# Optimization experiments

Hardware: AMD Instinct MI355X
Metric: run time of the kernel (lower is better)

The kernel has to match this reference:

```python
import jax, jax.numpy as jnp
import numpy as np
import math

NX = 4096   # input features (last_dim)
NY = 4096   # units
REDUCTION = 0.5  # param_reduction


def _make_window(nx, ny, reduction):
    """Faithful vectorized port of SzDense.build for form='diagonal', halfbandwidth=0."""
    hw = nx * ny / math.sqrt(nx * nx + ny * ny) * (1.0 - math.sqrt(reduction))
    rxy = (nx - 1) / (ny - 1)
    hwdiv = hw * math.sqrt(rxy * rxy + 1.0)
    iy = np.arange(ny, dtype=np.float64)
    c1 = rxy * iy - hwdiv
    # int(c1)+1 when c1>=0 (truncation == floor for nonneg), else 0
    ix1 = np.where(c1 >= 0, np.floor(c1).astype(np.int64) + 1, 0)
    c2 = rxy * iy + hwdiv
    ix2 = np.where(c2 < nx, np.ceil(c2).astype(np.int64), nx)
    ix = np.arange(nx)[:, None]
    wnd = ((ix >= ix1[None, :]) & (ix < ix2[None, :])).astype(np.float32)
    num_ones = float(wnd.sum())
    w_corr = (nx * ny) / num_ones if num_ones > 0 else 1.0
    return wnd, np.float32(w_corr)


def setup_inputs() -> dict:
    key = jax.random.key(0)
    kx, kk, kb = jax.random.split(key, 3)
    x = jax.random.normal(kx, (4096, NX), dtype=jnp.float32)
    wnd_np, w_corr = _make_window(NX, NY, REDUCTION)
    window = jnp.asarray(wnd_np)
    # glorot-uniform-like init, then build()'s kernel.assign(kernel * wnd * w_corr)
    limit = math.sqrt(6.0 / (NX + NY))
    kernel = jax.random.uniform(kk, (NX, NY), dtype=jnp.float32, minval=-limit, maxval=limit)
    kernel = kernel * window * w_corr
    bias = jnp.zeros((NY,), dtype=jnp.float32)
    return {"x": x, "kernel": kernel, "window": window, "bias": bias}


def reference(x, kernel, window, bias):
    # SzDense.call: dense(inputs, kernel * window, bias, activation=None)
    return jnp.matmul(x, kernel * window) + bias
```

## Files before the change

kernel.cpp:

```cpp
#include <hip/hip_runtime.h>
#include <hip/hip_bf16.h>
#include <stdint.h>

#define MM 4096
#define NN 4096
#define KK 4096
#define BM 128
#define BN 128
#define BK 32

typedef __bf16 bf16;
typedef __attribute__((ext_vector_type(8))) __bf16 bf16x8;
typedef __attribute__((ext_vector_type(4))) __bf16 bf16x4;
typedef __attribute__((ext_vector_type(4))) float f32x4;

__device__ inline const __attribute__((address_space(1))) void* to_global(const void* p) {
    return (const __attribute__((address_space(1))) void*)p;
}
__device__ inline __attribute__((address_space(3))) void* to_local(void* p) {
    return (__attribute__((address_space(3))) void*)p;
}

__global__ void convert_x(const float* __restrict__ x, bf16* __restrict__ out) {
    size_t i = ((size_t)blockIdx.x * blockDim.x + threadIdx.x) * 8;
    float4 v0 = *(const float4*)(x + i);
    float4 v1 = *(const float4*)(x + i + 4);
    bf16x8 o;
    o[0] = (bf16)v0.x; o[1] = (bf16)v0.y; o[2] = (bf16)v0.z; o[3] = (bf16)v0.w;
    o[4] = (bf16)v1.x; o[5] = (bf16)v1.y; o[6] = (bf16)v1.z; o[7] = (bf16)v1.w;
    *(bf16x8*)(out + i) = o;
}

#define LDN 68
__global__ void convert_wt(const float* __restrict__ w, const float* __restrict__ wnd,
                           bf16* __restrict__ bt) {
    __shared__ bf16 Ts[64][LDN];
    const int t = threadIdx.x;
    const int k0 = blockIdx.y * 64;
    const int n0 = blockIdx.x * 64;

    {
        const int nc = (t & 15) * 4;
        const int kb = t >> 4;
        #pragma unroll
        for (int p = 0; p < 4; ++p) {
            const int kl = p * 16 + kb;
            size_t idx = (size_t)(k0 + kl) * NN + (n0 + nc);
            float4 a = *(const float4*)(w + idx);
            float4 b = *(const float4*)(wnd + idx);
            bf16x4 o;
            o[0] = (bf16)(a.x * b.x);
            o[1] = (bf16)(a.y * b.y);
            o[2] = (bf16)(a.z * b.z);
            o[3] = (bf16)(a.w * b.w);
            *(bf16x4*)&Ts[kl][nc] = o;
        }
    }
    __syncthreads();

    {
        const int nl = t >> 2;
        #pragma unroll
        for (int p = 0; p < 2; ++p) {
            const int kc = (t & 3) + 4 * p;
            bf16x8 o;
            #pragma unroll
            for (int i = 0; i < 8; ++i) o[i] = Ts[kc * 8 + i][nl];
            *(bf16x8*)&bt[(size_t)(n0 + nl) * KK + k0 + kc * 8] = o;
        }
    }
}

__global__ __launch_bounds__(256, 3) void gemm_bt_bias(
    const bf16* __restrict__ A,
    const bf16* __restrict__ Bt,
    const float* __restrict__ bias,
    float* __restrict__ C) {
    __shared__ bf16 As[BM * BK];
    __shared__ bf16 Bs[BN * BK];

    const int t = threadIdx.x;
    const int wave = t >> 6;
    const int lane = t & 63;
    const int quad = lane >> 4;
    const int l15 = lane & 15;
    const int m0 = blockIdx.y * BM;
    const int n0 = blockIdx.x * BN;
    const int wm = wave >> 1;
    const int wn = wave & 1;

    f32x4 acc[4][4];
    #pragma unroll
    for (int i = 0; i < 4; ++i)
        #pragma unroll
        for (int j = 0; j < 4; ++j)
            acc[i][j] = (f32x4)0.0f;

    const int row_a0 = t >> 2;
    const int col_a0 = (t & 3) * 8;
    const bf16* Ag = A + (size_t)(m0 + row_a0) * KK + col_a0;
    const bf16* Bg = Bt + (size_t)(n0 + row_a0) * KK + col_a0;

    for (int k0 = 0; k0 < KK; k0 += BK) {
        #pragma unroll
        for (int c = 0; c < 2; ++c) {
            __builtin_amdgcn_global_load_lds(
                to_global(Ag + k0 + (size_t)c * 64 * KK),
                to_local(As + ((size_t)c * 256 + wave * 64) * 8), 16, 0, 0);
            __builtin_amdgcn_global_load_lds(
                to_global(Bg + k0 + (size_t)c * 64 * KK),
                to_local(Bs + ((size_t)c * 256 + wave * 64) * 8), 16, 0, 0);
        }
        __syncthreads();

        bf16x8 af[4], bfr[4];
        #pragma unroll
        for (int i = 0; i < 4; ++i)
            af[i] = *(const bf16x8*)&As[(wm * 64 + i * 16 + l15) * BK + quad * 8];
        #pragma unroll
        for (int j = 0; j < 4; ++j)
            bfr[j] = *(const bf16x8*)&Bs[(wn * 64 + j * 16 + l15) * BK + quad * 8];

        #pragma unroll
        for (int i = 0; i < 4; ++i)
            #pragma unroll
            for (int j = 0; j < 4; ++j)
                acc[i][j] = __builtin_amdgcn_mfma_f32_16x16x32_bf16(af[i], bfr[j], acc[i][j], 0, 0, 0);

        __syncthreads();
    }

    #pragma unroll
    for (int i = 0; i < 4; ++i) {
        #pragma unroll
        for (int j = 0; j < 4; ++j) {
            int col = n0 + wn * 64 + j * 16 + l15;
            float b = bias[col];
            #pragma unroll
            for (int r = 0; r < 4; ++r) {
                int row = m0 + wm * 64 + i * 16 + quad * 4 + r;
                C[(size_t)row * NN + col] = acc[i][j][r] + b;
            }
        }
    }
}

extern "C" void kernel_launch(void* const* d_in, const int* in_sizes, int n_in,
                              void* d_out, int out_size, void* d_ws, size_t ws_size,
                              hipStream_t stream) {
    const float* x = (const float*)d_in[0];
    const float* kern = (const float*)d_in[1];
    const float* wnd = (const float*)d_in[2];
    const float* bias = (const float*)d_in[3];
    float* out = (float*)d_out;

    bf16* Abf = (bf16*)d_ws;
    bf16* Btbf = (bf16*)((char*)d_ws + (size_t)MM * KK * sizeof(bf16));

    convert_x<<<(MM * (size_t)KK / 8 + 255) / 256, 256, 0, stream>>>(x, Abf);
    convert_wt<<<dim3(NN / 64, KK / 64), 256, 0, stream>>>(kern, wnd, Btbf);
    gemm_bt_bias<<<dim3(NN / BN, MM / BM), 256, 0, stream>>>(Abf, Btbf, bias, out);
}
```

Baseline: 360.9 us.

## Merge conversion kernels and remap GEMM tiles for per-XCD L2 locality

Merges the x conversion and the masked weight transpose into one launch, with the block index choosing which job each block does, which removes one kernel launch and the gap between launches. Remaps GEMM block indices so each XCD (blocks assigned round-robin by flat index) works on a contiguous group of four N tiles, so B tiles are reused within that XCD's L2. Raises the launch-bounds occupancy hint from 3 to 4 waves per SIMD, which may add register pressure or spills.

```diff
diff --git a/kernel.cpp b/kernel.cpp
--- a/kernel.cpp
+++ b/kernel.cpp
@@ -21,23 +21,29 @@
     return (__attribute__((address_space(3))) void*)p;
 }
 
-__global__ void convert_x(const float* __restrict__ x, bf16* __restrict__ out) {
-    size_t i = ((size_t)blockIdx.x * blockDim.x + threadIdx.x) * 8;
-    float4 v0 = *(const float4*)(x + i);
-    float4 v1 = *(const float4*)(x + i + 4);
-    bf16x8 o;
-    o[0] = (bf16)v0.x; o[1] = (bf16)v0.y; o[2] = (bf16)v0.z; o[3] = (bf16)v0.w;
-    o[4] = (bf16)v1.x; o[5] = (bf16)v1.y; o[6] = (bf16)v1.z; o[7] = (bf16)v1.w;
-    *(bf16x8*)(out + i) = o;
-}
-
 #define LDN 68
-__global__ void convert_wt(const float* __restrict__ w, const float* __restrict__ wnd,
-                           bf16* __restrict__ bt) {
+#define NBX 8192
+__global__ void prep(const float* __restrict__ x,
+                     const float* __restrict__ w,
+                     const float* __restrict__ wnd,
+                     bf16* __restrict__ Abf,
+                     bf16* __restrict__ bt) {
     __shared__ bf16 Ts[64][LDN];
     const int t = threadIdx.x;
-    const int k0 = blockIdx.y * 64;
-    const int n0 = blockIdx.x * 64;
+    int b = blockIdx.x;
+    if (b < NBX) {
+        size_t i = ((size_t)b * 256 + t) * 8;
+        float4 v0 = *(const float4*)(x + i);
+        float4 v1 = *(const float4*)(x + i + 4);
+        bf16x8 o;
+        o[0] = (bf16)v0.x; o[1] = (bf16)v0.y; o[2] = (bf16)v0.z; o[3] = (bf16)v0.w;
+        o[4] = (bf16)v1.x; o[5] = (bf16)v1.y; o[6] = (bf16)v1.z; o[7] = (bf16)v1.w;
+        *(bf16x8*)(Abf + i) = o;
+        return;
+    }
+    b -= NBX;
+    const int k0 = (b >> 6) * 64;
+    const int n0 = (b & 63) * 64;
 
     {
         const int nc = (t & 15) * 4;
@@ -47,12 +53,12 @@
             const int kl = p * 16 + kb;
             size_t idx = (size_t)(k0 + kl) * NN + (n0 + nc);
             float4 a = *(const float4*)(w + idx);
-            float4 b = *(const float4*)(wnd + idx);
+            float4 m = *(const float4*)(wnd + idx);
             bf16x4 o;
-            o[0] = (bf16)(a.x * b.x);
-            o[1] = (bf16)(a.y * b.y);
-            o[2] = (bf16)(a.z * b.z);
-            o[3] = (bf16)(a.w * b.w);
+            o[0] = (bf16)(a.x * m.x);
+            o[1] = (bf16)(a.y * m.y);
+            o[2] = (bf16)(a.z * m.z);
+            o[3] = (bf16)(a.w * m.w);
             *(bf16x4*)&Ts[kl][nc] = o;
         }
     }
@@ -71,7 +77,7 @@
     }
 }
 
-__global__ __launch_bounds__(256, 3) void gemm_bt_bias(
+__global__ __launch_bounds__(256, 4) void gemm_bt_bias(
     const bf16* __restrict__ A,
     const bf16* __restrict__ Bt,
     const float* __restrict__ bias,
@@ -84,8 +90,15 @@
     const int lane = t & 63;
     const int quad = lane >> 4;
     const int l15 = lane & 15;
-    const int m0 = blockIdx.y * BM;
-    const int n0 = blockIdx.x * BN;
+
+    const int flat = blockIdx.y * 32 + blockIdx.x;
+    const int xcd = flat & 7;
+    const int idx = flat >> 3;
+    const int n_tile = xcd * 4 + (idx & 3);
+    const int m_tile = idx >> 2;
+    const int m0 = m_tile * BM;
+    const int n0 = n_tile * BN;
+
     const int wm = wave >> 1;
     const int wn = wave & 1;
 
@@ -157,7 +170,6 @@
     bf16* Abf = (bf16*)d_ws;
     bf16* Btbf = (bf16*)((char*)d_ws + (size_t)MM * KK * sizeof(bf16));
 
-    convert_x<<<(MM * (size_t)KK / 8 + 255) / 256, 256, 0, stream>>>(x, Abf);
-    convert_wt<<<dim3(NN / 64, KK / 64), 256, 0, stream>>>(kern, wnd, Btbf);
-    gemm_bt_bias<<<dim3(NN / BN, MM / BM), 256, 0, stream>>>(Abf, Btbf, bias, out);
+    prep<<<NBX + (NN / 64) * (KK / 64), 256, 0, stream>>>(x, kern, wnd, Abf, Btbf);
+    gemm_bt_bias<<<dim3(32, 32), 256, 0, stream>>>(Abf, Btbf, bias, out);
 }
```

New measurement: 356.9 us. No clear change (-1.1%).
